# Kernel tuning notes

Measured on AMD Instinct MI355X. Metric: run time of the kernel, lower is better.

## Reference

```python
import jax, jax.numpy as jnp
import numpy as np

BLOCK = 32  # GGUF Q8_0 block size: one fp scale per 32 int8 quants


def setup_inputs() -> dict:
    key = jax.random.key(0)
    k1, k2, k3, k4 = jax.random.split(key, 4)
    O, I = 4096, 4096
    T = 8192  # tokens (batch*seq)
    x = jax.random.normal(k1, (T, I), dtype=jnp.float32)
    w_q = jax.random.randint(k2, (O, I), 0, 256, dtype=jnp.int32)
    scales = jax.random.uniform(k3, (O, I // BLOCK), dtype=jnp.float32) * 0.05 + 1e-3
    bias = jax.random.normal(k4, (O,), dtype=jnp.float32)
    return {"x": x, "w_q": w_q, "scales": scales, "bias": bias}


def _dequantize(w_q, scales, dtype):
    # Q8_0-style dequant: centered int quants * per-block scale.
    O, I = w_q.shape
    q = (w_q.astype(dtype) - 128.0).reshape(O, I // BLOCK, BLOCK)
    w = q * scales.astype(dtype)[:, :, None]  # [O, I/B, B]
    return w.reshape(O, I)


def reference(x, w_q, scales, bias):
    # cast_bias_weight: dequantize weight+bias to input dtype, then linear.
    dtype = x.dtype
    w = _dequantize(w_q, scales, dtype)          # [O, I]
    b = bias.astype(dtype)                       # [O]
    return jnp.einsum('ti,oi->to', x, w) + b     # [T, O]
```

## Files before the change

kernel.cpp:

```cpp
#include <hip/hip_runtime.h>

using bf16x8 = __attribute__((ext_vector_type(8))) __bf16;
using bf16x4 = __attribute__((ext_vector_type(4))) __bf16;
using f32x4  = __attribute__((ext_vector_type(4))) float;

#define BM 256
#define BN 256

__device__ __forceinline__ void async_load16(const void* g, void* l) {
    __builtin_amdgcn_global_load_lds(
        (const __attribute__((address_space(1))) unsigned int*)g,
        (__attribute__((address_space(3))) unsigned int*)l,
        16, 0, 0);
}

__global__ __launch_bounds__(256) void prep_x(
    const float* __restrict__ x, __bf16* __restrict__ xb, int n4) {
    const int c = blockIdx.x * 256 + threadIdx.x;
    if (c >= n4) return;
    const float4 a = ((const float4*)x)[c];
    bf16x4 v;
    v[0] = (__bf16)a.x; v[1] = (__bf16)a.y; v[2] = (__bf16)a.z; v[3] = (__bf16)a.w;
    ((bf16x4*)xb)[c] = v;
}

__global__ __launch_bounds__(256) void prep_w(
    const int* __restrict__ wq, const float* __restrict__ sc,
    __bf16* __restrict__ wb, int I) {
    const int row = blockIdx.y;
    const int c = blockIdx.x * 256 + threadIdx.x;
    const size_t base = (size_t)row * I + (size_t)c * 4;
    const float s = sc[row * (I >> 5) + (c >> 3)];
    const int4 a = *(const int4*)(wq + base);
    bf16x4 v;
    v[0] = (__bf16)((float)(a.x - 128) * s);
    v[1] = (__bf16)((float)(a.y - 128) * s);
    v[2] = (__bf16)((float)(a.z - 128) * s);
    v[3] = (__bf16)((float)(a.w - 128) * s);
    *(bf16x4*)(wb + base) = v;
}

#define REGA 0
#define REGB 65536

#define BARRIER()  __builtin_amdgcn_s_barrier()
#define LGKM0()    asm volatile("s_waitcnt lgkmcnt(0)" ::: "memory")
#define VMCNT4()   asm volatile("s_waitcnt vmcnt(4)" ::: "memory")
#define VMCNT0()   asm volatile("s_waitcnt vmcnt(0)" ::: "memory")
#define PRIO1()    __builtin_amdgcn_s_setprio(1)
#define PRIO0()    __builtin_amdgcn_s_setprio(0)

__global__ __launch_bounds__(512, 2) void gemm_8phase(
    const __bf16* __restrict__ A, const __bf16* __restrict__ B,
    const float* __restrict__ bias, float* __restrict__ C,
    int M, int N, int K) {
    __shared__ char lds[131072] __attribute__((aligned(16)));
    char* const ldsb = lds;

    const int tid  = threadIdx.x;
    const int wave = tid >> 6;
    const int lane = tid & 63;
    const int r = lane & 15;
    const int q = lane >> 4;
    const int wm = (wave >> 2) * 128;
    const int wn = (wave & 3) * 64;

    const int nwg = gridDim.x;
    const int q8 = nwg >> 3, r8 = nwg & 7;
    const int xcd = blockIdx.x & 7, seq = blockIdx.x >> 3;
    const int swz = (xcd < r8 ? xcd * (q8 + 1)
                              : r8 * (q8 + 1) + (xcd - r8) * q8) + seq;
    const int nTiles = N / BN;
    const int row0 = (swz / nTiles) * BM;
    const int col0 = (swz % nTiles) * BN;

    const size_t rowB = (size_t)K * sizeof(__bf16);

    const char* srcA[2];
    const char* srcB[2];
#pragma unroll
    for (int it = 0; it < 2; ++it) {
        const int p   = (it * 512 + tid) * 16;
        const int lin = p ^ (((p >> 7) & 7) << 4);
        const int gr  = lin >> 7;
        const int gc  = lin & 127;
        srcA[it] = (const char*)A + (size_t)(row0 + gr) * rowB + gc;
        srcB[it] = (const char*)B + (size_t)(col0 + gr) * rowB + gc;
    }

#define STAGE(mat, buf, ht, kb) do {                                         \
        async_load16(src##mat[0] + (size_t)(ht) * 128 * rowB + (kb),         \
            ldsb + REG##mat + (buf) * 32768 + (ht) * 16384 + wave * 1024);   \
        async_load16(src##mat[1] + (size_t)(ht) * 128 * rowB + (kb),         \
            ldsb + REG##mat + (buf) * 32768 + (ht) * 16384 + 8192 + wave * 1024); \
    } while (0)

    const int sb0 = (q ^ (r & 7)) * 16;
    const int sb1 = ((4 + q) ^ (r & 7)) * 16;
    const int aBase = REGA + (wm + r) * 128;
    const int bBase = REGB + (wn + r) * 128;

    bf16x8 afr[4][2];
    bf16x8 bfr[4][2];
    f32x4  acc[8][4];
    const f32x4 zero = {0.f, 0.f, 0.f, 0.f};
#pragma unroll
    for (int i = 0; i < 8; ++i)
#pragma unroll
        for (int j = 0; j < 4; ++j) acc[i][j] = zero;

#define LDA4(buf, mb) do { _Pragma("unroll")                                 \
        for (int mm = 0; mm < 4; ++mm) {                                     \
            const char* pa = ldsb + (buf) * 32768 + aBase + ((mb) + mm) * 2048; \
            afr[mm][0] = *(const bf16x8*)(pa + sb0);                         \
            afr[mm][1] = *(const bf16x8*)(pa + sb1);                         \
        } } while (0)

#define LDB2(buf, nb) do { _Pragma("unroll")                                 \
        for (int nn = 0; nn < 2; ++nn) {                                     \
            const char* pb = ldsb + (buf) * 32768 + bBase + ((nb) + nn) * 2048; \
            bfr[(nb) + nn][0] = *(const bf16x8*)(pb + sb0);                  \
            bfr[(nb) + nn][1] = *(const bf16x8*)(pb + sb1);                  \
        } } while (0)

#define QUAD(mb, nb) do { _Pragma("unroll")                                  \
        for (int mm = 0; mm < 4; ++mm) { _Pragma("unroll")                   \
        for (int nn = 0; nn < 2; ++nn) { _Pragma("unroll")                   \
        for (int ks = 0; ks < 2; ++ks)                                       \
            acc[(mb) + mm][(nb) + nn] = __builtin_amdgcn_mfma_f32_16x16x32_bf16( \
                afr[mm][ks], bfr[(nb) + nn][ks], acc[(mb) + mm][(nb) + nn], 0, 0, 0); \
        } } } while (0)

    STAGE(A, 0, 0, 0);   STAGE(A, 0, 1, 0);
    STAGE(B, 0, 0, 0);   STAGE(B, 0, 1, 0);
    STAGE(A, 1, 0, 128); STAGE(A, 1, 1, 128);
    VMCNT4();
    BARRIER();

    const int nIter = K >> 7;
    for (int i = 0; i < nIter; ++i) {
        const int k0 = i << 7;
        const size_t kb1 = (size_t)(k0 + 64) * 2;
        int k2 = k0 + 128; if (k2 >= K) k2 -= K;
        int k3 = k0 + 192; if (k3 >= K) k3 -= K;
        const size_t kb2 = (size_t)k2 * 2;
        const size_t kb3 = (size_t)k3 * 2;

        LDA4(0, 0); LDB2(0, 0);
        STAGE(B, 1, 0, kb1); STAGE(B, 1, 1, kb1);
        BARRIER(); LGKM0();
        PRIO1(); QUAD(0, 0); PRIO0();
        BARRIER();
        LDB2(0, 2);
        BARRIER(); LGKM0();
        PRIO1(); QUAD(0, 2); PRIO0();
        BARRIER();
        LDA4(0, 4);
        BARRIER(); LGKM0();
        PRIO1(); QUAD(4, 2); PRIO0();
        BARRIER();
        STAGE(A, 0, 0, kb2); STAGE(A, 0, 1, kb2);
        BARRIER(); LGKM0();
        PRIO1(); QUAD(4, 0); PRIO0();
        VMCNT4();
        BARRIER();
        LDA4(1, 0); LDB2(1, 0);
        STAGE(B, 0, 0, kb2); STAGE(B, 0, 1, kb2);
        BARRIER(); LGKM0();
        PRIO1(); QUAD(0, 0); PRIO0();
        BARRIER();
        LDB2(1, 2);
        BARRIER(); LGKM0();
        PRIO1(); QUAD(0, 2); PRIO0();
        BARRIER();
        LDA4(1, 4);
        BARRIER(); LGKM0();
        PRIO1(); QUAD(4, 2); PRIO0();
        BARRIER();
        STAGE(A, 1, 0, kb3); STAGE(A, 1, 1, kb3);
        BARRIER(); LGKM0();
        PRIO1(); QUAD(4, 0); PRIO0();
        VMCNT4();
        BARRIER();
    }

    VMCNT0();

#pragma unroll
    for (int n = 0; n < 4; ++n) {
        const int col = col0 + wn + n * 16 + r;
        const float bv = bias[col];
#pragma unroll
        for (int m = 0; m < 8; ++m) {
            const int row = row0 + wm + m * 16 + q * 4;
#pragma unroll
            for (int e = 0; e < 4; ++e)
                C[(size_t)(row + e) * N + col] = acc[m][n][e] + bv;
        }
    }
}

__global__ void fallback_kernel(
    const float* __restrict__ x, const int* __restrict__ wq,
    const float* __restrict__ sc, const float* __restrict__ bias,
    float* __restrict__ out, int T, int O, int I) {
    int o = blockIdx.x * 16 + threadIdx.x;
    int t = blockIdx.y * 16 + threadIdx.y;
    if (o >= O || t >= T) return;
    const int nb = I >> 5;
    float s = 0.f;
    for (int b = 0; b < nb; ++b) {
        const float scv = sc[o * nb + b];
        float p = 0.f;
        for (int k = 0; k < 32; ++k)
            p += x[(size_t)t * I + b * 32 + k] *
                 (float)(wq[(size_t)o * I + b * 32 + k] - 128);
        s += scv * p;
    }
    out[(size_t)t * O + o] = s + bias[o];
}

extern "C" void kernel_launch(void* const* d_in, const int* in_sizes, int n_in,
                              void* d_out, int out_size, void* d_ws, size_t ws_size,
                              hipStream_t stream) {
    const float* x    = (const float*)d_in[0];
    const int*   wq   = (const int*)d_in[1];
    const float* sc   = (const float*)d_in[2];
    const float* bias = (const float*)d_in[3];
    float* out = (float*)d_out;

    const long long xn = in_sizes[0];
    const long long wn = in_sizes[1];
    const int O = in_sizes[3];
    const int I = (int)(wn / O);
    const int T = (int)(xn / I);

    const size_t xbBytes = (size_t)T * I * sizeof(__bf16);
    const size_t wbBytes = (size_t)O * I * sizeof(__bf16);

    const bool fast = (ws_size >= xbBytes + wbBytes) &&
                      (T % BM == 0) && (O % BN == 0) && (I % 1024 == 0) &&
                      (((long long)T * I) % 1024 == 0);

    if (!fast) {
        dim3 blk(16, 16);
        dim3 grd((O + 15) / 16, (T + 15) / 16);
        hipLaunchKernelGGL(fallback_kernel, grd, blk, 0, stream,
                           x, wq, sc, bias, out, T, O, I);
        return;
    }

    __bf16* xb = (__bf16*)d_ws;
    __bf16* wb = (__bf16*)((char*)d_ws + xbBytes);

    {
        const int n4 = (int)((long long)T * I / 4);
        hipLaunchKernelGGL(prep_x, dim3((n4 + 255) / 256), dim3(256), 0, stream,
                           x, xb, n4);
        hipLaunchKernelGGL(prep_w, dim3(I / 1024, O), dim3(256), 0, stream,
                           wq, sc, wb, I);
    }
    const int nwg = (T / BM) * (O / BN);
    hipLaunchKernelGGL(gemm_8phase, dim3(nwg), dim3(512), 0, stream,
                       xb, wb, bias, out, T, O, I);
}
```

Baseline: 511.6 us.

## Fuse bf16 conversion and Q8 dequant into GEMM register-staged loads

Removes the separate prep_x and prep_w kernels and their bf16 workspace round-trip. The GEMM now loads fp32 activations and int32 quants straight from global memory into registers, converts and dequantizes them, and writes bf16 to LDS inside the 8-phase pipeline. The async global-to-LDS loads are replaced by register staging. In exchange, each tile re-reads fp32 and int32 data, which is twice the bytes of bf16, across many workgroups. It also adds VGPR pressure and conversion ALU work inside the MFMA loop.

```diff
diff --git a/kernel.cpp b/kernel.cpp
--- a/kernel.cpp
+++ b/kernel.cpp
@@ -1,59 +1,23 @@
 #include <hip/hip_runtime.h>
 
 using bf16x8 = __attribute__((ext_vector_type(8))) __bf16;
-using bf16x4 = __attribute__((ext_vector_type(4))) __bf16;
 using f32x4  = __attribute__((ext_vector_type(4))) float;
 
 #define BM 256
 #define BN 256
 
-__device__ __forceinline__ void async_load16(const void* g, void* l) {
-    __builtin_amdgcn_global_load_lds(
-        (const __attribute__((address_space(1))) unsigned int*)g,
-        (__attribute__((address_space(3))) unsigned int*)l,
-        16, 0, 0);
-}
-
-__global__ __launch_bounds__(256) void prep_x(
-    const float* __restrict__ x, __bf16* __restrict__ xb, int n4) {
-    const int c = blockIdx.x * 256 + threadIdx.x;
-    if (c >= n4) return;
-    const float4 a = ((const float4*)x)[c];
-    bf16x4 v;
-    v[0] = (__bf16)a.x; v[1] = (__bf16)a.y; v[2] = (__bf16)a.z; v[3] = (__bf16)a.w;
-    ((bf16x4*)xb)[c] = v;
-}
-
-__global__ __launch_bounds__(256) void prep_w(
-    const int* __restrict__ wq, const float* __restrict__ sc,
-    __bf16* __restrict__ wb, int I) {
-    const int row = blockIdx.y;
-    const int c = blockIdx.x * 256 + threadIdx.x;
-    const size_t base = (size_t)row * I + (size_t)c * 4;
-    const float s = sc[row * (I >> 5) + (c >> 3)];
-    const int4 a = *(const int4*)(wq + base);
-    bf16x4 v;
-    v[0] = (__bf16)((float)(a.x - 128) * s);
-    v[1] = (__bf16)((float)(a.y - 128) * s);
-    v[2] = (__bf16)((float)(a.z - 128) * s);
-    v[3] = (__bf16)((float)(a.w - 128) * s);
-    *(bf16x4*)(wb + base) = v;
-}
-
 #define REGA 0
 #define REGB 65536
 
 #define BARRIER()  __builtin_amdgcn_s_barrier()
 #define LGKM0()    asm volatile("s_waitcnt lgkmcnt(0)" ::: "memory")
-#define VMCNT4()   asm volatile("s_waitcnt vmcnt(4)" ::: "memory")
-#define VMCNT0()   asm volatile("s_waitcnt vmcnt(0)" ::: "memory")
 #define PRIO1()    __builtin_amdgcn_s_setprio(1)
 #define PRIO0()    __builtin_amdgcn_s_setprio(0)
 
-__global__ __launch_bounds__(512, 2) void gemm_8phase(
-    const __bf16* __restrict__ A, const __bf16* __restrict__ B,
-    const float* __restrict__ bias, float* __restrict__ C,
-    int M, int N, int K) {
+__global__ __launch_bounds__(512, 2) void gemm_fused(
+    const float* __restrict__ x, const int* __restrict__ wq,
+    const float* __restrict__ sc, const float* __restrict__ bias,
+    float* __restrict__ C, int M, int N, int K) {
     __shared__ char lds[131072] __attribute__((aligned(16)));
     char* const ldsb = lds;
 
@@ -74,26 +38,65 @@
     const int row0 = (swz / nTiles) * BM;
     const int col0 = (swz % nTiles) * BN;
 
-    const size_t rowB = (size_t)K * sizeof(__bf16);
-
-    const char* srcA[2];
-    const char* srcB[2];
+    const int nsb = K >> 5;
+
+    const float* srcAx[2];
+    const int*   srcWq[2];
+    int scRow[2], keOff[2];
 #pragma unroll
     for (int it = 0; it < 2; ++it) {
         const int p   = (it * 512 + tid) * 16;
         const int lin = p ^ (((p >> 7) & 7) << 4);
         const int gr  = lin >> 7;
-        const int gc  = lin & 127;
-        srcA[it] = (const char*)A + (size_t)(row0 + gr) * rowB + gc;
-        srcB[it] = (const char*)B + (size_t)(col0 + gr) * rowB + gc;
-    }
-
-#define STAGE(mat, buf, ht, kb) do {                                         \
-        async_load16(src##mat[0] + (size_t)(ht) * 128 * rowB + (kb),         \
-            ldsb + REG##mat + (buf) * 32768 + (ht) * 16384 + wave * 1024);   \
-        async_load16(src##mat[1] + (size_t)(ht) * 128 * rowB + (kb),         \
-            ldsb + REG##mat + (buf) * 32768 + (ht) * 16384 + 8192 + wave * 1024); \
-    } while (0)
+        const int gcE = (lin & 127) >> 1;
+        srcAx[it] = x  + (size_t)(row0 + gr) * K + gcE;
+        srcWq[it] = wq + (size_t)(col0 + gr) * K + gcE;
+        scRow[it] = (col0 + gr) * nsb;
+        keOff[it] = gcE;
+    }
+
+#define ISSUE_A(V, ht, ke) do { _Pragma("unroll")                            \
+        for (int it = 0; it < 2; ++it) {                                     \
+            const float* s_ = srcAx[it] + (size_t)(ht) * 128 * K + (ke);     \
+            V[it][0] = *(const float4*)s_;                                   \
+            V[it][1] = *(const float4*)(s_ + 4);                             \
+        } } while (0)
+
+#define ISSUE_B(V, S, ht, ke) do { _Pragma("unroll")                         \
+        for (int it = 0; it < 2; ++it) {                                     \
+            const int* s_ = srcWq[it] + (size_t)(ht) * 128 * K + (ke);       \
+            V[it][0] = *(const int4*)s_;                                     \
+            V[it][1] = *(const int4*)(s_ + 4);                               \
+            S[it] = sc[scRow[it] + (ht) * 128 * nsb                          \
+                       + (((ke) + keOff[it]) >> 5)];                         \
+        } } while (0)
+
+#define COMMIT_A(V, buf, ht) do { _Pragma("unroll")                          \
+        for (int it = 0; it < 2; ++it) {                                     \
+            bf16x8 v;                                                        \
+            v[0] = (__bf16)V[it][0].x; v[1] = (__bf16)V[it][0].y;            \
+            v[2] = (__bf16)V[it][0].z; v[3] = (__bf16)V[it][0].w;            \
+            v[4] = (__bf16)V[it][1].x; v[5] = (__bf16)V[it][1].y;            \
+            v[6] = (__bf16)V[it][1].z; v[7] = (__bf16)V[it][1].w;            \
+            *(bf16x8*)(ldsb + REGA + (buf) * 32768 + (ht) * 16384            \
+                       + (it * 512 + tid) * 16) = v;                         \
+        } } while (0)
+
+#define COMMIT_B(V, S, buf, ht) do { _Pragma("unroll")                       \
+        for (int it = 0; it < 2; ++it) {                                     \
+            const float s_ = S[it];                                          \
+            bf16x8 v;                                                        \
+            v[0] = (__bf16)((float)(V[it][0].x - 128) * s_);                 \
+            v[1] = (__bf16)((float)(V[it][0].y - 128) * s_);                 \
+            v[2] = (__bf16)((float)(V[it][0].z - 128) * s_);                 \
+            v[3] = (__bf16)((float)(V[it][0].w - 128) * s_);                 \
+            v[4] = (__bf16)((float)(V[it][1].x - 128) * s_);                 \
+            v[5] = (__bf16)((float)(V[it][1].y - 128) * s_);                 \
+            v[6] = (__bf16)((float)(V[it][1].z - 128) * s_);                 \
+            v[7] = (__bf16)((float)(V[it][1].w - 128) * s_);                 \
+            *(bf16x8*)(ldsb + REGB + (buf) * 32768 + (ht) * 16384            \
+                       + (it * 512 + tid) * 16) = v;                         \
+        } } while (0)
 
     const int sb0 = (q ^ (r & 7)) * 16;
     const int sb1 = ((4 + q) ^ (r & 7)) * 16;
@@ -131,60 +134,72 @@
                 afr[mm][ks], bfr[(nb) + nn][ks], acc[(mb) + mm][(nb) + nn], 0, 0, 0); \
         } } } while (0)
 
-    STAGE(A, 0, 0, 0);   STAGE(A, 0, 1, 0);
-    STAGE(B, 0, 0, 0);   STAGE(B, 0, 1, 0);
-    STAGE(A, 1, 0, 128); STAGE(A, 1, 1, 128);
-    VMCNT4();
+    float4 vA0[2][2], vA1[2][2];
+    int4   vB0[2][2], vB1[2][2];
+    float  sB0v[2], sB1v[2];
+
+    ISSUE_A(vA0, 0, 0);        ISSUE_A(vA1, 1, 0);
+    ISSUE_B(vB0, sB0v, 0, 0);  ISSUE_B(vB1, sB1v, 1, 0);
+    COMMIT_A(vA0, 0, 0);       COMMIT_A(vA1, 0, 1);
+    COMMIT_B(vB0, sB0v, 0, 0); COMMIT_B(vB1, sB1v, 0, 1);
+    ISSUE_B(vB0, sB0v, 0, 64); ISSUE_B(vB1, sB1v, 1, 64);
+    LGKM0();
     BARRIER();
 
     const int nIter = K >> 7;
     for (int i = 0; i < nIter; ++i) {
-        const int k0 = i << 7;
-        const size_t kb1 = (size_t)(k0 + 64) * 2;
-        int k2 = k0 + 128; if (k2 >= K) k2 -= K;
-        int k3 = k0 + 192; if (k3 >= K) k3 -= K;
-        const size_t kb2 = (size_t)k2 * 2;
-        const size_t kb3 = (size_t)k3 * 2;
-
+        const int ke0 = i << 7;
+        const int ke1 = ke0 + 64;
+        int ke2 = ke0 + 128; if (ke2 >= K) ke2 -= K;
+        int ke3 = ke0 + 192; if (ke3 >= K) ke3 -= K;
+
+        ISSUE_A(vA0, 0, ke1);
         LDA4(0, 0); LDB2(0, 0);
-        STAGE(B, 1, 0, kb1); STAGE(B, 1, 1, kb1);
+        COMMIT_B(vB0, sB0v, 1, 0);
         BARRIER(); LGKM0();
         PRIO1(); QUAD(0, 0); PRIO0();
         BARRIER();
+        ISSUE_A(vA1, 1, ke1);
         LDB2(0, 2);
+        COMMIT_B(vB1, sB1v, 1, 1);
         BARRIER(); LGKM0();
         PRIO1(); QUAD(0, 2); PRIO0();
         BARRIER();
+        ISSUE_B(vB0, sB0v, 0, ke2);
         LDA4(0, 4);
+        COMMIT_A(vA0, 1, 0);
         BARRIER(); LGKM0();
         PRIO1(); QUAD(4, 2); PRIO0();
         BARRIER();
-        STAGE(A, 0, 0, kb2); STAGE(A, 0, 1, kb2);
+        ISSUE_B(vB1, sB1v, 1, ke2);
+        COMMIT_A(vA1, 1, 1);
         BARRIER(); LGKM0();
         PRIO1(); QUAD(4, 0); PRIO0();
-        VMCNT4();
-        BARRIER();
+        BARRIER();
+        ISSUE_A(vA0, 0, ke2);
         LDA4(1, 0); LDB2(1, 0);
-        STAGE(B, 0, 0, kb2); STAGE(B, 0, 1, kb2);
+        COMMIT_B(vB0, sB0v, 0, 0);
         BARRIER(); LGKM0();
         PRIO1(); QUAD(0, 0); PRIO0();
         BARRIER();
+        ISSUE_A(vA1, 1, ke2);
         LDB2(1, 2);
+        COMMIT_B(vB1, sB1v, 0, 1);
         BARRIER(); LGKM0();
         PRIO1(); QUAD(0, 2); PRIO0();
         BARRIER();
+        ISSUE_B(vB0, sB0v, 0, ke3);
         LDA4(1, 4);
+        COMMIT_A(vA0, 0, 0);
         BARRIER(); LGKM0();
         PRIO1(); QUAD(4, 2); PRIO0();
         BARRIER();
-        STAGE(A, 1, 0, kb3); STAGE(A, 1, 1, kb3);
+        ISSUE_B(vB1, sB1v, 1, ke3);
+        COMMIT_A(vA1, 0, 1);
         BARRIER(); LGKM0();
         PRIO1(); QUAD(4, 0); PRIO0();
-        VMCNT4();
-        BARRIER();
-    }
-
-    VMCNT0();
+        BARRIER();
+    }
 
 #pragma unroll
     for (int n = 0; n < 4; ++n) {
@@ -235,12 +250,7 @@
     const int I = (int)(wn / O);
     const int T = (int)(xn / I);
 
-    const size_t xbBytes = (size_t)T * I * sizeof(__bf16);
-    const size_t wbBytes = (size_t)O * I * sizeof(__bf16);
-
-    const bool fast = (ws_size >= xbBytes + wbBytes) &&
-                      (T % BM == 0) && (O % BN == 0) && (I % 1024 == 0) &&
-                      (((long long)T * I) % 1024 == 0);
+    const bool fast = (T % BM == 0) && (O % BN == 0) && (I % 128 == 0);
 
     if (!fast) {
         dim3 blk(16, 16);
@@ -250,17 +260,7 @@
         return;
     }
 
-    __bf16* xb = (__bf16*)d_ws;
-    __bf16* wb = (__bf16*)((char*)d_ws + xbBytes);
-
-    {
-        const int n4 = (int)((long long)T * I / 4);
-        hipLaunchKernelGGL(prep_x, dim3((n4 + 255) / 256), dim3(256), 0, stream,
-                           x, xb, n4);
-        hipLaunchKernelGGL(prep_w, dim3(I / 1024, O), dim3(256), 0, stream,
-                           wq, sc, wb, I);
-    }
     const int nwg = (T / BM) * (O / BN);
-    hipLaunchKernelGGL(gemm_8phase, dim3(nwg), dim3(512), 0, stream,
-                       xb, wb, bias, out, T, O, I);
+    hipLaunchKernelGGL(gemm_fused, dim3(nwg), dim3(512), 0, stream,
+                       x, wq, sc, bias, out, T, O, I);
 }
```

Measured after the change: 1.733 ms. +238.8%, slower.
